# Performance work log

Hardware: AMD Instinct MI355X
Metric: run time of the kernel (lower is better)

Reference implementation:

```python
import jax, jax.numpy as jnp
import numpy as np

N, M, NNZ, D, H = 4096, 1024, 65536, 512, 8
DH = D // H
DFF = 4 * D
EPS = 1e-5


def layer_norm(x, g, b):
    mu = jnp.mean(x, axis=-1, keepdims=True)
    var = jnp.mean((x - mu) ** 2, axis=-1, keepdims=True)
    return (x - mu) / jnp.sqrt(var + EPS) * g + b


def setup_inputs() -> dict:
    key = jax.random.key(0)
    ks = jax.random.split(key, 16)
    s = 1.0 / np.sqrt(D)
    inp = {}
    inp['x'] = jax.random.normal(ks[0], (N, D), jnp.float32)
    node = jax.random.randint(ks[1], (NNZ,), 0, N, jnp.int32)
    edge = jax.random.randint(ks[2], (NNZ,), 0, M, jnp.int32)
    inp['hyperedge_index'] = jnp.stack([node, edge], axis=0)
    inp['hyperedge_attr'] = jax.random.normal(ks[3], (M, D), jnp.float32)
    # HypergraphConv params (heads=1): lin (no bias), att [2*D], output bias
    inp['Wh'] = jax.random.normal(ks[4], (D, D), jnp.float32) * s
    inp['att'] = jax.random.normal(ks[5], (2 * D,), jnp.float32) * s
    inp['bias_h'] = jnp.zeros((D,), jnp.float32)
    # outer LayerNorms
    inp['ln1_g'] = jnp.ones((D,), jnp.float32); inp['ln1_b'] = jnp.zeros((D,), jnp.float32)
    inp['ln2_g'] = jnp.ones((D,), jnp.float32); inp['ln2_b'] = jnp.zeros((D,), jnp.float32)
    # TransformerEncoderLayer params (post-norm, relu, dropout off at eval)
    inp['in_proj_w'] = jax.random.normal(ks[6], (3 * D, D), jnp.float32) * s
    inp['in_proj_b'] = jnp.zeros((3 * D,), jnp.float32)
    inp['out_proj_w'] = jax.random.normal(ks[7], (D, D), jnp.float32) * s
    inp['out_proj_b'] = jnp.zeros((D,), jnp.float32)
    inp['ff1_w'] = jax.random.normal(ks[8], (DFF, D), jnp.float32) * s
    inp['ff1_b'] = jnp.zeros((DFF,), jnp.float32)
    inp['ff2_w'] = jax.random.normal(ks[9], (D, DFF), jnp.float32) * (1.0 / np.sqrt(DFF))
    inp['ff2_b'] = jnp.zeros((D,), jnp.float32)
    inp['tln1_g'] = jnp.ones((D,), jnp.float32); inp['tln1_b'] = jnp.zeros((D,), jnp.float32)
    inp['tln2_g'] = jnp.ones((D,), jnp.float32); inp['tln2_b'] = jnp.zeros((D,), jnp.float32)
    return inp


def hypergraph_conv(x, node, edge, hyperedge_attr, Wh, att, bias_h):
    # PyG HypergraphConv, use_attention=True, heads=1, concat=True
    xl = x @ Wh.T                      # [N, D]
    el = hyperedge_attr @ Wh.T         # [M, D]
    # per-incidence attention score
    a = xl[node] @ att[:D] + el[edge] @ att[D:]          # [NNZ]
    a = jnp.where(a >= 0, a, 0.2 * a)                    # leaky_relu(0.2)
    # scatter-softmax grouped by node index
    amax = jax.ops.segment_max(a, node, num_segments=N)
    a = jnp.exp(a - amax[node])
    den = jax.ops.segment_sum(a, node, num_segments=N)
    alpha = a / (den[node] + 1e-16)
    # degree normalizations (hyperedge_weight = ones)
    ones = jnp.ones((NNZ,), x.dtype)
    Dn = jax.ops.segment_sum(ones, node, num_segments=N)
    Dinv = jnp.where(Dn > 0, 1.0 / Dn, 0.0)
    Bn = jax.ops.segment_sum(ones, edge, num_segments=M)
    Binv = jnp.where(Bn > 0, 1.0 / Bn, 0.0)
    # node -> hyperedge aggregation
    msg1 = (Binv[edge] * alpha)[:, None] * xl[node]      # [NNZ, D]
    ef = jax.ops.segment_sum(msg1, edge, num_segments=M)  # [M, D]
    # hyperedge -> node aggregation
    msg2 = (Dinv[node] * alpha)[:, None] * ef[edge]
    out = jax.ops.segment_sum(msg2, node, num_segments=N)  # [N, D]
    return out + bias_h


def reference(x, hyperedge_index, hyperedge_attr, Wh, att, bias_h,
              ln1_g, ln1_b, ln2_g, ln2_b,
              in_proj_w, in_proj_b, out_proj_w, out_proj_b,
              ff1_w, ff1_b, ff2_w, ff2_b,
              tln1_g, tln1_b, tln2_g, tln2_b):
    node, edge = hyperedge_index[0], hyperedge_index[1]
    x_conv = hypergraph_conv(x, node, edge, hyperedge_attr, Wh, att, bias_h)
    x1 = layer_norm(x + x_conv, ln1_g, ln1_b)
    # TransformerEncoderLayer (post-norm, eval: dropout off), seq of N tokens
    qkv = x1 @ in_proj_w.T + in_proj_b
    q, k, v = jnp.split(qkv, 3, axis=-1)
    q = q.reshape(N, H, DH); k = k.reshape(N, H, DH); v = v.reshape(N, H, DH)
    scores = jnp.einsum('nhd,mhd->hnm', q, k) / np.sqrt(DH)
    attw = jax.nn.softmax(scores, axis=-1)
    ctx = jnp.einsum('hnm,mhd->nhd', attw, v).reshape(N, D)
    attn_out = ctx @ out_proj_w.T + out_proj_b
    x2 = layer_norm(x1 + attn_out, tln1_g, tln1_b)
    ff = jax.nn.relu(x2 @ ff1_w.T + ff1_b) @ ff2_w.T + ff2_b
    x3 = layer_norm(x2 + ff, tln2_g, tln2_b)
    return layer_norm(x1 + x3, ln2_g, ln2_b)
```

## Files before the change

kernel.cpp:

```cpp
#include <hip/hip_runtime.h>
#include <math.h>

#define NN   4096
#define MM   1024
#define NNZC 65536
#define DD   512
#define HH   8
#define DHH  64
#define DFFC 2048
#define NSPLIT 8

typedef short bf16x8 __attribute__((ext_vector_type(8)));
typedef float f32x4  __attribute__((ext_vector_type(4)));

static __device__ inline unsigned short f2bf(float f) {
  union { float f; unsigned int u; } v; v.f = f;
  unsigned int r = v.u + 0x7fff + ((v.u >> 16) & 1);
  return (unsigned short)(r >> 16);
}
static __device__ inline float bf2f(unsigned short u) {
  return __uint_as_float((unsigned int)u << 16);
}

__device__ inline void gload16(const void* g, void* l) {
  __builtin_amdgcn_global_load_lds(
      (const __attribute__((address_space(1))) void*)g,
      (__attribute__((address_space(3))) void*)l, 16, 0, 0);
}

__device__ inline void atomicMaxF(float* addr, float val) {
  if (val >= 0.f) atomicMax((int*)addr, __float_as_int(val));
  else            atomicMin((unsigned int*)addr, __float_as_uint(val));
}

__global__ void init_kernel(float* amax, float* den, int* DnCnt, int* BnCnt,
                            int* node_cur, int* edge_cur) {
  int i = blockIdx.x * 256 + threadIdx.x;
  if (i < NN) { amax[i] = -INFINITY; den[i] = 0.f; DnCnt[i] = 0; node_cur[i] = 0; }
  if (i < MM) { BnCnt[i] = 0; edge_cur[i] = 0; }
}

__global__ __launch_bounds__(256) void f2b_multi(
    const float* s0, unsigned short* d0, int n0,
    const float* s1, unsigned short* d1, int n1,
    const float* s2, unsigned short* d2, int n2,
    const float* s3, unsigned short* d3, int n3,
    const float* s4, unsigned short* d4, int n4,
    const float* s5, unsigned short* d5, int n5,
    const float* s6, unsigned short* d6, int n6) {
  const float* in; unsigned short* out; int n8;
  switch (blockIdx.y) {
    case 0: in=s0; out=d0; n8=n0; break;
    case 1: in=s1; out=d1; n8=n1; break;
    case 2: in=s2; out=d2; n8=n2; break;
    case 3: in=s3; out=d3; n8=n3; break;
    case 4: in=s4; out=d4; n8=n4; break;
    case 5: in=s5; out=d5; n8=n5; break;
    default: in=s6; out=d6; n8=n6; break;
  }
  for (int i = blockIdx.x*256 + threadIdx.x; i < n8; i += gridDim.x*256) {
    float4 v0 = *(const float4*)&in[(size_t)i*8];
    float4 v1 = *(const float4*)&in[(size_t)i*8 + 4];
    unsigned short w[8];
    w[0]=f2bf(v0.x); w[1]=f2bf(v0.y); w[2]=f2bf(v0.z); w[3]=f2bf(v0.w);
    w[4]=f2bf(v1.x); w[5]=f2bf(v1.y); w[6]=f2bf(v1.z); w[7]=f2bf(v1.w);
    *(ulonglong2*)&out[(size_t)i*8] = *(ulonglong2*)w;
  }
}

__global__ __launch_bounds__(256) void gemm_bt_bf16(
    const unsigned short* __restrict__ A, const unsigned short* __restrict__ B,
    const float* __restrict__ bias, float* __restrict__ Cf,
    unsigned short* __restrict__ Cb, int N, int K, int relu) {
  __shared__ __align__(16) unsigned short Al[128*64];
  __shared__ __align__(16) unsigned short Bl[128*64];
  const int t = threadIdx.x;
  const int w = t >> 6, l = t & 63;
  const int lg = l >> 4, lid = l & 15;
  const int wr = w >> 1, wc = w & 1;
  const int bm = blockIdx.x * 128, bn = blockIdx.y * 128;

  f32x4 acc[4][4];
  #pragma unroll
  for (int mi = 0; mi < 4; ++mi)
    #pragma unroll
    for (int ni = 0; ni < 4; ++ni) acc[mi][ni] = (f32x4)0.f;

  for (int k0 = 0; k0 < K; k0 += 64) {
    #pragma unroll
    for (int i = 0; i < 4; ++i) {
      int cid = i*256 + t;
      int row = cid >> 3, cp = cid & 7;
      int gc = cp ^ (row & 7);
      gload16(&A[(size_t)(bm + row)*K + k0 + gc*8], &Al[cid*8]);
      gload16(&B[(size_t)(bn + row)*K + k0 + gc*8], &Bl[cid*8]);
    }
    asm volatile("s_waitcnt vmcnt(0)" ::: "memory");
    __syncthreads();
    #pragma unroll
    for (int ks = 0; ks < 2; ++ks) {
      bf16x8 af[4], bfr[4];
      #pragma unroll
      for (int mi = 0; mi < 4; ++mi) {
        int r = wr*64 + mi*16 + lid;
        af[mi] = *(const bf16x8*)&Al[r*64 + ((ks*4 + lg) ^ (r & 7))*8];
      }
      #pragma unroll
      for (int ni = 0; ni < 4; ++ni) {
        int r = wc*64 + ni*16 + lid;
        bfr[ni] = *(const bf16x8*)&Bl[r*64 + ((ks*4 + lg) ^ (r & 7))*8];
      }
      __builtin_amdgcn_s_setprio(1);
      #pragma unroll
      for (int mi = 0; mi < 4; ++mi)
        #pragma unroll
        for (int ni = 0; ni < 4; ++ni)
          acc[mi][ni] = __builtin_amdgcn_mfma_f32_16x16x32_bf16(af[mi], bfr[ni], acc[mi][ni], 0, 0, 0);
      __builtin_amdgcn_s_setprio(0);
    }
    __syncthreads();
  }

  #pragma unroll
  for (int ni = 0; ni < 4; ++ni) {
    int col = bn + wc*64 + ni*16 + lid;
    float bv = bias ? bias[col] : 0.f;
    #pragma unroll
    for (int mi = 0; mi < 4; ++mi) {
      #pragma unroll
      for (int rg = 0; rg < 4; ++rg) {
        int row = bm + wr*64 + mi*16 + lg*4 + rg;
        float v = acc[mi][ni][rg] + bv;
        if (relu) v = fmaxf(v, 0.f);
        if (Cf) Cf[(size_t)row*N + col] = v;
        if (Cb) Cb[(size_t)row*N + col] = f2bf(v);
      }
    }
  }
}

__global__ __launch_bounds__(256) void gemm_bt_bf16_n64(
    const unsigned short* __restrict__ A, const unsigned short* __restrict__ B,
    const float* __restrict__ bias, unsigned short* __restrict__ Cb, int N, int K,
    unsigned short* __restrict__ VtbOpt) {
  __shared__ __align__(16) unsigned short Al[128*64];
  __shared__ __align__(16) unsigned short Bl[64*64];
  const int t = threadIdx.x;
  const int w = t >> 6, l = t & 63;
  const int lg = l >> 4, lid = l & 15;
  const int wr = w >> 1, wc = w & 1;
  const int bm = blockIdx.x * 128, bn = blockIdx.y * 64;

  f32x4 acc[4][2];
  #pragma unroll
  for (int mi = 0; mi < 4; ++mi)
    #pragma unroll
    for (int ni = 0; ni < 2; ++ni) acc[mi][ni] = (f32x4)0.f;

  for (int k0 = 0; k0 < K; k0 += 64) {
    #pragma unroll
    for (int i = 0; i < 4; ++i) {
      int cid = i*256 + t;
      int row = cid >> 3, cp = cid & 7;
      int gc = cp ^ (row & 7);
      gload16(&A[(size_t)(bm + row)*K + k0 + gc*8], &Al[cid*8]);
    }
    #pragma unroll
    for (int i = 0; i < 2; ++i) {
      int cid = i*256 + t;
      int row = cid >> 3, cp = cid & 7;
      int gc = cp ^ (row & 7);
      gload16(&B[(size_t)(bn + row)*K + k0 + gc*8], &Bl[cid*8]);
    }
    asm volatile("s_waitcnt vmcnt(0)" ::: "memory");
    __syncthreads();
    #pragma unroll
    for (int ks = 0; ks < 2; ++ks) {
      bf16x8 af[4], bfr[2];
      #pragma unroll
      for (int mi = 0; mi < 4; ++mi) {
        int r = wr*64 + mi*16 + lid;
        af[mi] = *(const bf16x8*)&Al[r*64 + ((ks*4 + lg) ^ (r & 7))*8];
      }
      #pragma unroll
      for (int ni = 0; ni < 2; ++ni) {
        int r = wc*32 + ni*16 + lid;
        bfr[ni] = *(const bf16x8*)&Bl[r*64 + ((ks*4 + lg) ^ (r & 7))*8];
      }
      __builtin_amdgcn_s_setprio(1);
      #pragma unroll
      for (int mi = 0; mi < 4; ++mi)
        #pragma unroll
        for (int ni = 0; ni < 2; ++ni)
          acc[mi][ni] = __builtin_amdgcn_mfma_f32_16x16x32_bf16(af[mi], bfr[ni], acc[mi][ni], 0, 0, 0);
      __builtin_amdgcn_s_setprio(0);
    }
    __syncthreads();
  }

  if (VtbOpt && bn >= 1024) {
    #pragma unroll
    for (int ni = 0; ni < 2; ++ni) {
      int col = bn + wc*32 + ni*16 + lid;
      float bv = bias ? bias[col] : 0.f;
      int d = col - 1024;
      int h = d >> 6, dd = d & 63;
      #pragma unroll
      for (int mi = 0; mi < 4; ++mi) {
        int tok0 = bm + wr*64 + mi*16 + lg*4;
        ushort4 w4;
        w4.x = f2bf(acc[mi][ni][0] + bv);
        w4.y = f2bf(acc[mi][ni][1] + bv);
        w4.z = f2bf(acc[mi][ni][2] + bv);
        w4.w = f2bf(acc[mi][ni][3] + bv);
        *(ushort4*)&VtbOpt[(size_t)h*64*NN + (size_t)dd*NN + tok0] = w4;
      }
    }
  } else {
    #pragma unroll
    for (int ni = 0; ni < 2; ++ni) {
      int col = bn + wc*32 + ni*16 + lid;
      float bv = bias ? bias[col] : 0.f;
      #pragma unroll
      for (int mi = 0; mi < 4; ++mi) {
        #pragma unroll
        for (int rg = 0; rg < 4; ++rg) {
          int row = bm + wr*64 + mi*16 + lg*4 + rg;
          Cb[(size_t)row*N + col] = f2bf(acc[mi][ni][rg] + bv);
        }
      }
    }
  }
}

__global__ __launch_bounds__(256) void rowdot_both(const unsigned short* __restrict__ xlb,
    const unsigned short* __restrict__ elb, const float* __restrict__ att,
    float* __restrict__ s_node, float* __restrict__ s_edge) {
  int w = (blockIdx.x * 256 + threadIdx.x) >> 6;
  int lane = threadIdx.x & 63;
  const unsigned short* xr;
  const float* vec;
  if (w < NN) { xr = &xlb[(size_t)w * DD]; vec = att; }
  else        { xr = &elb[(size_t)(w - NN) * DD]; vec = att + DD; }
  float s = 0.f;
  #pragma unroll
  for (int j = 0; j < 8; ++j) s += bf2f(xr[lane + 64*j]) * vec[lane + 64*j];
  #pragma unroll
  for (int off = 1; off < 64; off <<= 1) s += __shfl_xor(s, off, 64);
  if (lane == 0) {
    if (w < NN) s_node[w] = s;
    else        s_edge[w - NN] = s;
  }
}

__global__ void incidence_pass1(const int* __restrict__ node_idx, const int* __restrict__ edge_idx,
    const float* __restrict__ s_node, const float* __restrict__ s_edge,
    float* __restrict__ a_buf, float* amax, int* DnCnt, int* BnCnt) {
  int i = blockIdx.x * 256 + threadIdx.x;
  if (i >= NNZC) return;
  int n = node_idx[i], m = edge_idx[i];
  float a = s_node[n] + s_edge[m];
  a = (a >= 0.f) ? a : 0.2f * a;
  a_buf[i] = a;
  atomicMaxF(&amax[n], a);
  atomicAdd(&DnCnt[n], 1);
  atomicAdd(&BnCnt[m], 1);
}

__global__ __launch_bounds__(1024) void exscan2_kernel(const int* __restrict__ inA,
    int* __restrict__ outA, int nA, const int* __restrict__ inB, int* __restrict__ outB, int nB) {
  const int* in; int* out; int n;
  if (blockIdx.x == 0) { in = inA; out = outA; n = nA; }
  else                 { in = inB; out = outB; n = nB; }
  __shared__ int sums[1024];
  const int t = threadIdx.x;
  const int chunk = (n + 1023) >> 10;
  const int start = t * chunk;
  const int stop  = min(start + chunk, n);
  int local = 0;
  for (int i = start; i < stop; ++i) local += in[i];
  sums[t] = local;
  __syncthreads();
  for (int o = 1; o < 1024; o <<= 1) {
    int v = (t >= o) ? sums[t - o] : 0;
    __syncthreads();
    sums[t] += v;
    __syncthreads();
  }
  int run = (t == 0) ? 0 : sums[t - 1];
  for (int i = start; i < stop; ++i) { out[i] = run; run += in[i]; }
  if (t == 1023) out[n] = sums[1023];
}

__global__ void incidence_pass2(const int* __restrict__ node_idx, const int* __restrict__ edge_idx,
    float* __restrict__ a_buf, const float* __restrict__ amax, float* den,
    const int* __restrict__ node_off, const int* __restrict__ edge_off,
    int* node_cur, int* edge_cur, int* node_list, int* edge_list) {
  int i = blockIdx.x * 256 + threadIdx.x;
  if (i >= NNZC) return;
  int n = node_idx[i], m = edge_idx[i];
  float e = __expf(a_buf[i] - amax[n]);
  a_buf[i] = e;
  atomicAdd(&den[n], e);
  int pn = atomicAdd(&node_cur[n], 1);
  node_list[node_off[n] + pn] = i;
  int pm = atomicAdd(&edge_cur[m], 1);
  edge_list[edge_off[m] + pm] = i;
}

__global__ __launch_bounds__(256) void gather_edge(const int* __restrict__ edge_off,
    const int* __restrict__ edge_list, const int* __restrict__ node_idx,
    const float* __restrict__ a_buf, const float* __restrict__ den,
    const unsigned short* __restrict__ xlb, unsigned short* __restrict__ efb) {
  int m = blockIdx.x;
  int t = threadIdx.x;
  int beg = edge_off[m], end = edge_off[m+1];
  int cnt = end - beg;
  float Binv = (cnt > 0) ? (1.0f / (float)cnt) : 0.f;
  __shared__ int   ln_[128];
  __shared__ float lw_[128];
  float acc0 = 0.f, acc1 = 0.f;
  for (int c = beg; c < end; c += 128) {
    int nchunk = min(128, end - c);
    if (t < nchunk) {
      int i = edge_list[c + t];
      int n = node_idx[i];
      ln_[t] = n;
      lw_[t] = a_buf[i] / (den[n] + 1e-16f) * Binv;
    }
    __syncthreads();
    float a0 = 0.f, a1 = 0.f, b0 = 0.f, b1 = 0.f;
    int j = 0;
    for (; j + 1 < nchunk; j += 2) {
      float w0 = lw_[j], w1 = lw_[j+1];
      const unsigned short* r0 = &xlb[(size_t)ln_[j]   * DD];
      const unsigned short* r1 = &xlb[(size_t)ln_[j+1] * DD];
      a0 += w0 * bf2f(r0[t]);       b0 += w0 * bf2f(r0[t + 256]);
      a1 += w1 * bf2f(r1[t]);       b1 += w1 * bf2f(r1[t + 256]);
    }
    if (j < nchunk) {
      float w0 = lw_[j];
      const unsigned short* r0 = &xlb[(size_t)ln_[j] * DD];
      a0 += w0 * bf2f(r0[t]);       b0 += w0 * bf2f(r0[t + 256]);
    }
    acc0 += a0 + a1;
    acc1 += b0 + b1;
    __syncthreads();
  }
  efb[(size_t)m * DD + t]       = f2bf(acc0);
  efb[(size_t)m * DD + t + 256] = f2bf(acc1);
}

__global__ __launch_bounds__(256) void gather_node_ln(const int* __restrict__ node_off,
    const int* __restrict__ node_list, const int* __restrict__ edge_idx,
    const float* __restrict__ a_buf, const float* __restrict__ den,
    const unsigned short* __restrict__ efb, const float* __restrict__ bias_h,
    const float* __restrict__ x, const float* __restrict__ g, const float* __restrict__ be,
    float* __restrict__ x1, unsigned short* __restrict__ x1b) {
  int n = blockIdx.x;
  int t = threadIdx.x;
  int beg = node_off[n], end = node_off[n+1];
  int cnt = end - beg;
  float Dinv = (cnt > 0) ? (1.0f / (float)cnt) : 0.f;
  float wscale = Dinv / (den[n] + 1e-16f);
  __shared__ int   le_[128];
  __shared__ float lw_[128];
  float acc0 = 0.f, acc1 = 0.f;
  for (int c = beg; c < end; c += 128) {
    int nchunk = min(128, end - c);
    if (t < nchunk) {
      int i = node_list[c + t];
      le_[t] = edge_idx[i];
      lw_[t] = a_buf[i] * wscale;
    }
    __syncthreads();
    float a0 = 0.f, a1 = 0.f, b0 = 0.f, b1 = 0.f;
    int j = 0;
    for (; j + 1 < nchunk; j += 2) {
      float w0 = lw_[j], w1 = lw_[j+1];
      const unsigned short* r0 = &efb[(size_t)le_[j]   * DD];
      const unsigned short* r1 = &efb[(size_t)le_[j+1] * DD];
      a0 += w0 * bf2f(r0[t]);       b0 += w0 * bf2f(r0[t + 256]);
      a1 += w1 * bf2f(r1[t]);       b1 += w1 * bf2f(r1[t + 256]);
    }
    if (j < nchunk) {
      float w0 = lw_[j];
      const unsigned short* r0 = &efb[(size_t)le_[j] * DD];
      a0 += w0 * bf2f(r0[t]);       b0 += w0 * bf2f(r0[t + 256]);
    }
    acc0 += a0 + a1;
    acc1 += b0 + b1;
    __syncthreads();
  }
  float v0 = x[(size_t)n*DD + t]       + acc0 + bias_h[t];
  float v1 = x[(size_t)n*DD + t + 256] + acc1 + bias_h[t + 256];
  __shared__ float red[4];
  __shared__ float mu_s, rstd_s;
  float s = v0 + v1;
  #pragma unroll
  for (int off = 1; off < 64; off <<= 1) s += __shfl_xor(s, off, 64);
  int wid = t >> 6;
  if ((t & 63) == 0) red[wid] = s;
  __syncthreads();
  if (t == 0) mu_s = (red[0] + red[1] + red[2] + red[3]) / 512.f;
  __syncthreads();
  float mu = mu_s;
  float d0 = v0 - mu, d1 = v1 - mu;
  float vs = d0*d0 + d1*d1;
  #pragma unroll
  for (int off = 1; off < 64; off <<= 1) vs += __shfl_xor(vs, off, 64);
  if ((t & 63) == 0) red[wid] = vs;
  __syncthreads();
  if (t == 0) rstd_s = rsqrtf((red[0] + red[1] + red[2] + red[3]) / 512.f + 1e-5f);
  __syncthreads();
  float rs = rstd_s;
  float o0 = d0 * rs * g[t]       + be[t];
  float o1 = d1 * rs * g[t + 256] + be[t + 256];
  x1[(size_t)n*DD + t]        = o0;
  x1[(size_t)n*DD + t + 256]  = o1;
  x1b[(size_t)n*DD + t]       = f2bf(o0);
  x1b[(size_t)n*DD + t + 256] = f2bf(o1);
}

__global__ __launch_bounds__(256) void ln_residual(const float* __restrict__ a,
    const float* __restrict__ b, const unsigned short* __restrict__ bB,
    const float* __restrict__ g, const float* __restrict__ be,
    float* __restrict__ out, unsigned short* __restrict__ outb) {
  int r = blockIdx.x;
  int t = threadIdx.x;
  float b0 = b ? b[(size_t)r*DD + t]       : bf2f(bB[(size_t)r*DD + t]);
  float b1 = b ? b[(size_t)r*DD + t + 256] : bf2f(bB[(size_t)r*DD + t + 256]);
  float v0 = a[(size_t)r*DD + t]       + b0;
  float v1 = a[(size_t)r*DD + t + 256] + b1;
  __shared__ float red[4];
  __shared__ float mu_s, rstd_s;
  float s = v0 + v1;
  #pragma unroll
  for (int off = 1; off < 64; off <<= 1) s += __shfl_xor(s, off, 64);
  int wid = t >> 6;
  if ((t & 63) == 0) red[wid] = s;
  __syncthreads();
  if (t == 0) mu_s = (red[0] + red[1] + red[2] + red[3]) / 512.f;
  __syncthreads();
  float mu = mu_s;
  float d0 = v0 - mu, d1 = v1 - mu;
  float vs = d0*d0 + d1*d1;
  #pragma unroll
  for (int off = 1; off < 64; off <<= 1) vs += __shfl_xor(vs, off, 64);
  if ((t & 63) == 0) red[wid] = vs;
  __syncthreads();
  if (t == 0) rstd_s = rsqrtf((red[0] + red[1] + red[2] + red[3]) / 512.f + 1e-5f);
  __syncthreads();
  float rs = rstd_s;
  float o0 = d0 * rs * g[t]       + be[t];
  float o1 = d1 * rs * g[t + 256] + be[t + 256];
  out[(size_t)r*DD + t]       = o0;
  out[(size_t)r*DD + t + 256] = o1;
  if (outb) {
    outb[(size_t)r*DD + t]       = f2bf(o0);
    outb[(size_t)r*DD + t + 256] = f2bf(o1);
  }
}

__global__ __launch_bounds__(256) void ln_final2(const float* __restrict__ x2,
    const unsigned short* __restrict__ ffob, const float* __restrict__ x1,
    const float* __restrict__ g1, const float* __restrict__ b1,
    const float* __restrict__ g2, const float* __restrict__ b2,
    float* __restrict__ out) {
  int r = blockIdx.x;
  int t = threadIdx.x;
  __shared__ float red[4];
  __shared__ float sh0, sh1;
  int wid = t >> 6;
  float v0 = x2[(size_t)r*DD + t]       + bf2f(ffob[(size_t)r*DD + t]);
  float v1 = x2[(size_t)r*DD + t + 256] + bf2f(ffob[(size_t)r*DD + t + 256]);
  float s = v0 + v1;
  #pragma unroll
  for (int off = 1; off < 64; off <<= 1) s += __shfl_xor(s, off, 64);
  if ((t & 63) == 0) red[wid] = s;
  __syncthreads();
  if (t == 0) sh0 = (red[0] + red[1] + red[2] + red[3]) / 512.f;
  __syncthreads();
  float mu = sh0;
  float d0 = v0 - mu, d1 = v1 - mu;
  float vs = d0*d0 + d1*d1;
  #pragma unroll
  for (int off = 1; off < 64; off <<= 1) vs += __shfl_xor(vs, off, 64);
  if ((t & 63) == 0) red[wid] = vs;
  __syncthreads();
  if (t == 0) sh1 = rsqrtf((red[0] + red[1] + red[2] + red[3]) / 512.f + 1e-5f);
  __syncthreads();
  float rs = sh1;
  float x30 = d0 * rs * g1[t]       + b1[t];
  float x31 = d1 * rs * g1[t + 256] + b1[t + 256];
  __syncthreads();
  float u0 = x1[(size_t)r*DD + t]       + x30;
  float u1 = x1[(size_t)r*DD + t + 256] + x31;
  s = u0 + u1;
  #pragma unroll
  for (int off = 1; off < 64; off <<= 1) s += __shfl_xor(s, off, 64);
  if ((t & 63) == 0) red[wid] = s;
  __syncthreads();
  if (t == 0) sh0 = (red[0] + red[1] + red[2] + red[3]) / 512.f;
  __syncthreads();
  mu = sh0;
  d0 = u0 - mu; d1 = u1 - mu;
  vs = d0*d0 + d1*d1;
  #pragma unroll
  for (int off = 1; off < 64; off <<= 1) vs += __shfl_xor(vs, off, 64);
  if ((t & 63) == 0) red[wid] = vs;
  __syncthreads();
  if (t == 0) sh1 = rsqrtf((red[0] + red[1] + red[2] + red[3]) / 512.f + 1e-5f);
  __syncthreads();
  rs = sh1;
  out[(size_t)r*DD + t]       = d0 * rs * g2[t]       + b2[t];
  out[(size_t)r*DD + t + 256] = d1 * rs * g2[t + 256] + b2[t + 256];
}

__global__ __launch_bounds__(256) void attn_mfma_part(const unsigned short* __restrict__ qkvbb,
                                                      const unsigned short* __restrict__ Vtb,
                                                      unsigned short* __restrict__ Opartb,
                                                      float* __restrict__ ml) {
  const int head = blockIdx.y;
  const int z = blockIdx.z;
  const int q0 = blockIdx.x * 64;
  const int t = threadIdx.x;
  const int w = t >> 6;
  const int l = t & 63;
  const int lg = l >> 4;
  const int lid = l & 15;
  const float sc = 0.125f * 1.44269504f;
  const float THRraw = 44.36f;

  __shared__ __align__(16) unsigned short Kl[64*64];
  __shared__ __align__(16) unsigned short Vl[64*64];

  bf16x8 qa[2];
  {
    const int qrow = q0 + w*16 + lid;
    const unsigned short* qp = &qkvbb[(size_t)qrow*1536 + head*64];
    qa[0] = *(const bf16x8*)&qp[lg*8];
    qa[1] = *(const bf16x8*)&qp[32 + lg*8];
  }

  float m = -1e30f, msc = -1e30f, lsum = 0.f;
  f32x4 o[4];
  #pragma unroll
  for (int dt = 0; dt < 4; ++dt) o[dt] = (f32x4)0.f;

  const unsigned short* Kh = qkvbb + 512 + head*64;
  const unsigned short* Vh = Vtb + (size_t)head*64*NN;
  const int kt0 = z * (NN / NSPLIT);
  const int kt1 = kt0 + (NN / NSPLIT);

  const int srow0 = t >> 3,        scc = (t & 7) * 8;
  const int srow1 = 32 + (t >> 3);
  const int sdst0 = (srow0*64 + scc) ^ ((srow0 & 7) << 3);
  const int sdst1 = (srow1*64 + scc) ^ ((srow1 & 7) << 3);
  const int kperm0 = 8*((srow0>>2)&3) + 4*((srow0>>4)&1) + (srow0&3) + 32*(srow0>>5);
  const int kperm1 = 8*((srow1>>2)&3) + 4*((srow1>>4)&1) + (srow1&3) + 32*(srow1>>5);
  ulonglong2 kreg0, kreg1, vreg0, vreg1;

#define LOADKV(ktv) do { \
    kreg0 = *(const ulonglong2*)&Kh[(size_t)((ktv) + kperm0)*1536 + scc]; \
    vreg0 = *(const ulonglong2*)&Vh[(size_t)srow0*NN + (ktv) + scc]; \
    kreg1 = *(const ulonglong2*)&Kh[(size_t)((ktv) + kperm1)*1536 + scc]; \
    vreg1 = *(const ulonglong2*)&Vh[(size_t)srow1*NN + (ktv) + scc]; \
  } while (0)
#define STORKV() do { \
    *(ulonglong2*)&Kl[sdst0] = kreg0; *(ulonglong2*)&Vl[sdst0] = vreg0; \
    *(ulonglong2*)&Kl[sdst1] = kreg1; *(ulonglong2*)&Vl[sdst1] = vreg1; \
  } while (0)

  LOADKV(kt0);
  STORKV();
  __syncthreads();

  for (int kt = kt0; kt < kt1; kt += 64) {
    const bool hn = (kt + 64) < kt1;
    if (hn) LOADKV(kt + 64);

    f32x4 s[4];
    #pragma unroll
    for (int n = 0; n < 4; ++n) s[n] = (f32x4)0.f;
    __builtin_amdgcn_s_setprio(1);
    #pragma unroll
    for (int n = 0; n < 4; ++n) {
      int tok = n*16 + lid;
      #pragma unroll
      for (int hf = 0; hf < 2; ++hf) {
        int didx = (tok*64 + hf*32 + lg*8) ^ ((tok & 7) << 3);
        bf16x8 kb = *(const bf16x8*)&Kl[didx];
        s[n] = __builtin_amdgcn_mfma_f32_16x16x32_bf16(kb, qa[hf], s[n], 0, 0, 0);
      }
    }
    __builtin_amdgcn_s_setprio(0);

    float a0 = fmaxf(fmaxf(s[0][0], s[0][1]), s[0][2]);
    float a1 = fmaxf(fmaxf(s[0][3], s[1][0]), s[1][1]);
    float a2 = fmaxf(fmaxf(s[1][2], s[1][3]), s[2][0]);
    float a3 = fmaxf(fmaxf(s[2][1], s[2][2]), s[2][3]);
    float a4 = fmaxf(fmaxf(s[3][0], s[3][1]), s[3][2]);
    float mx = fmaxf(fmaxf(fmaxf(a0, a1), a2), fmaxf(fmaxf(a3, a4), s[3][3]));
    mx = fmaxf(mx, __shfl_xor(mx, 16, 64));
    mx = fmaxf(mx, __shfl_xor(mx, 32, 64));
    if (!__all(mx <= m + THRraw)) {
      float mn = fmaxf(m, mx);
      float c = exp2f((m - mn) * sc);
      m = mn;
      msc = m * sc;
      lsum *= c;
      #pragma unroll
      for (int r = 0; r < 4; ++r) {
        float cr = __shfl(c, lg*4 + r, 64);
        #pragma unroll
        for (int dt = 0; dt < 4; ++dt) o[dt][r] *= cr;
      }
    }
    float ps = 0.f;
    #pragma unroll
    for (int n = 0; n < 4; ++n)
      #pragma unroll
      for (int r = 0; r < 4; ++r) {
        float p = exp2f(fmaf(s[n][r], sc, -msc));
        s[n][r] = p;
        ps += p;
      }
    ps += __shfl_xor(ps, 16, 64);
    ps += __shfl_xor(ps, 32, 64);
    lsum += ps;

    union { bf16x8 v; unsigned int u[4]; } pa[2];
    #pragma unroll
    for (int hf = 0; hf < 2; ++hf) {
      asm("v_cvt_pk_bf16_f32 %0, %1, %2" : "=v"(pa[hf].u[0]) : "v"(s[2*hf][0]),   "v"(s[2*hf][1]));
      asm("v_cvt_pk_bf16_f32 %0, %1, %2" : "=v"(pa[hf].u[1]) : "v"(s[2*hf][2]),   "v"(s[2*hf][3]));
      asm("v_cvt_pk_bf16_f32 %0, %1, %2" : "=v"(pa[hf].u[2]) : "v"(s[2*hf+1][0]), "v"(s[2*hf+1][1]));
      asm("v_cvt_pk_bf16_f32 %0, %1, %2" : "=v"(pa[hf].u[3]) : "v"(s[2*hf+1][2]), "v"(s[2*hf+1][3]));
    }

    __builtin_amdgcn_s_setprio(1);
    #pragma unroll
    for (int dt = 0; dt < 4; ++dt) {
      int drow = dt*16 + lid;
      #pragma unroll
      for (int hf = 0; hf < 2; ++hf) {
        int didx = (drow*64 + hf*32 + lg*8) ^ ((drow & 7) << 3);
        bf16x8 vb = *(const bf16x8*)&Vl[didx];
        o[dt] = __builtin_amdgcn_mfma_f32_16x16x32_bf16(pa[hf].v, vb, o[dt], 0, 0, 0);
      }
    }
    __builtin_amdgcn_s_setprio(0);

    __syncthreads();
    if (hn) {
      STORKV();
      __syncthreads();
    }
  }
#undef LOADKV
#undef STORKV

  #pragma unroll
  for (int r = 0; r < 4; ++r) {
    int q = q0 + w*16 + lg*4 + r;
    size_t base = ((size_t)(z*HH + head)*NN + q)*64;
    #pragma unroll
    for (int dt = 0; dt < 4; ++dt)
      Opartb[base + dt*16 + lid] = f2bf(o[dt][r]);
  }
  if (l < 16) {
    int q = q0 + w*16 + l;
    size_t mb = ((size_t)(z*HH + head)*NN + q)*2;
    ml[mb]     = msc;
    ml[mb + 1] = lsum;
  }
}

__global__ __launch_bounds__(256) void attn_combine(const unsigned short* __restrict__ Opartb,
                                                    const float* __restrict__ ml,
                                                    unsigned short* __restrict__ ctxb) {
  const int w = threadIdx.x >> 6, lane = threadIdx.x & 63;
  const int row = blockIdx.x * 4 + w;
  const int q = row >> 3, head = row & 7;
  float ms[NSPLIT], ls[NSPLIT];
  float mglob = -1e30f;
  #pragma unroll
  for (int s = 0; s < NSPLIT; ++s) {
    size_t mb = ((size_t)(s*HH + head)*NN + q)*2;
    ms[s] = ml[mb]; ls[s] = ml[mb + 1];
    mglob = fmaxf(mglob, ms[s]);
  }
  float lt = 0.f, ov = 0.f;
  #pragma unroll
  for (int s = 0; s < NSPLIT; ++s) {
    float wgt = exp2f(ms[s] - mglob);
    lt += ls[s] * wgt;
    ov += bf2f(Opartb[((size_t)(s*HH + head)*NN + q)*64 + lane]) * wgt;
  }
  ctxb[(size_t)q*DD + head*64 + lane] = f2bf(ov / lt);
}

extern "C" void kernel_launch(void* const* d_in, const int* in_sizes, int n_in,
                              void* d_out, int out_size, void* d_ws, size_t ws_size,
                              hipStream_t stream) {
  const float* x       = (const float*)d_in[0];
  const int*   hidx    = (const int*)d_in[1];
  const float* hattr   = (const float*)d_in[2];
  const float* Wh      = (const float*)d_in[3];
  const float* att     = (const float*)d_in[4];
  const float* bias_h  = (const float*)d_in[5];
  const float* ln1_g   = (const float*)d_in[6];
  const float* ln1_b   = (const float*)d_in[7];
  const float* ln2_g   = (const float*)d_in[8];
  const float* ln2_b   = (const float*)d_in[9];
  const float* in_proj_w  = (const float*)d_in[10];
  const float* in_proj_b  = (const float*)d_in[11];
  const float* out_proj_w = (const float*)d_in[12];
  const float* out_proj_b = (const float*)d_in[13];
  const float* ff1_w   = (const float*)d_in[14];
  const float* ff1_b   = (const float*)d_in[15];
  const float* ff2_w   = (const float*)d_in[16];
  const float* ff2_b   = (const float*)d_in[17];
  const float* tln1_g  = (const float*)d_in[18];
  const float* tln1_b  = (const float*)d_in[19];
  const float* tln2_g  = (const float*)d_in[20];
  const float* tln2_b  = (const float*)d_in[21];
  const int* node_idx = hidx;
  const int* edge_idx = hidx + NNZC;

  char* ws = (char*)d_ws;
  size_t off = 0;
  auto alloc = [&](size_t bytes) -> void* {
    void* p = ws + off;
    off = (off + bytes + 63) & ~(size_t)63;
    return p;
  };
  float* s_node   = (float*)alloc(sizeof(float)*NN);
  float* s_edge   = (float*)alloc(sizeof(float)*MM);
  float* a_buf    = (float*)alloc(sizeof(float)*NNZC);
  float* amax     = (float*)alloc(sizeof(float)*NN);
  float* den      = (float*)alloc(sizeof(float)*NN);
  int*   DnCnt    = (int*)alloc(sizeof(int)*NN);
  int*   BnCnt    = (int*)alloc(sizeof(int)*MM);
  int*   node_off = (int*)alloc(sizeof(int)*(NN+1));
  int*   edge_off = (int*)alloc(sizeof(int)*(MM+1));
  int*   node_cur = (int*)alloc(sizeof(int)*NN);
  int*   edge_cur = (int*)alloc(sizeof(int)*MM);
  int*   node_list= (int*)alloc(sizeof(int)*NNZC);
  int*   edge_list= (int*)alloc(sizeof(int)*NNZC);
  float* x1       = (float*)alloc(sizeof(float)*NN*DD);
  float* x2       = (float*)alloc(sizeof(float)*NN*DD);
  unsigned short* xhb   = (unsigned short*)alloc(sizeof(unsigned short)*(NN+MM)*DD);
  unsigned short* xelb  = (unsigned short*)alloc(sizeof(unsigned short)*(NN+MM)*DD);
  unsigned short* efb   = (unsigned short*)alloc(sizeof(unsigned short)*MM*DD);
  unsigned short* qkvbb = (unsigned short*)alloc(sizeof(unsigned short)*NN*3*DD);
  unsigned short* Vtb   = (unsigned short*)alloc(sizeof(unsigned short)*NN*DD);
  unsigned short* Whb   = (unsigned short*)alloc(sizeof(unsigned short)*DD*DD);
  unsigned short* ipwb  = (unsigned short*)alloc(sizeof(unsigned short)*3*DD*DD);
  unsigned short* opwb  = (unsigned short*)alloc(sizeof(unsigned short)*DD*DD);
  unsigned short* ff1wb = (unsigned short*)alloc(sizeof(unsigned short)*DFFC*DD);
  unsigned short* ff2wb = (unsigned short*)alloc(sizeof(unsigned short)*DD*DFFC);
  unsigned short* x1b   = (unsigned short*)alloc(sizeof(unsigned short)*NN*DD);
  unsigned short* x2b   = (unsigned short*)alloc(sizeof(unsigned short)*NN*DD);
  unsigned short* ctxb  = (unsigned short*)alloc(sizeof(unsigned short)*NN*DD);
  unsigned short* attn_outb = (unsigned short*)alloc(sizeof(unsigned short)*NN*DD);
  char* late = (char*)alloc(34u*1024*1024);
  unsigned short* Opartb = (unsigned short*)late;
  float*          mlb    = (float*)(late + 32u*1024*1024);
  unsigned short* ffhb   = (unsigned short*)late;
  unsigned short* ffob   = (unsigned short*)(late + 16u*1024*1024);
  unsigned short* xlb = xelb;
  unsigned short* elb = xelb + (size_t)NN*DD;
  (void)ws_size; (void)in_sizes; (void)n_in; (void)out_size;

  dim3 b256(256);
  f2b_multi<<<dim3(256, 7), b256, 0, stream>>>(
      x, xhb, NN*DD/8,  hattr, xhb + (size_t)NN*DD, MM*DD/8,  Wh, Whb, DD*DD/8,
      in_proj_w, ipwb, 3*DD*DD/8,  out_proj_w, opwb, DD*DD/8,
      ff1_w, ff1wb, DFFC*DD/8,  ff2_w, ff2wb, DD*DFFC/8);

  gemm_bt_bf16_n64<<<dim3((NN+MM)/128, DD/64), b256, 0, stream>>>(xhb, Whb, nullptr, xelb, DD, DD, nullptr);
  rowdot_both<<<(NN+MM)/4, b256, 0, stream>>>(xlb, elb, att, s_node, s_edge);
  init_kernel<<<NN/256, b256, 0, stream>>>(amax, den, DnCnt, BnCnt, node_cur, edge_cur);
  incidence_pass1<<<NNZC/256, b256, 0, stream>>>(node_idx, edge_idx, s_node, s_edge,
                                                 a_buf, amax, DnCnt, BnCnt);
  exscan2_kernel<<<2, 1024, 0, stream>>>(DnCnt, node_off, NN, BnCnt, edge_off, MM);
  incidence_pass2<<<NNZC/256, b256, 0, stream>>>(node_idx, edge_idx, a_buf, amax, den,
                                                 node_off, edge_off, node_cur, edge_cur,
                                                 node_list, edge_list);
  gather_edge<<<MM, b256, 0, stream>>>(edge_off, edge_list, node_idx, a_buf, den, xlb, efb);
  gather_node_ln<<<NN, b256, 0, stream>>>(node_off, node_list, edge_idx, a_buf, den, efb,
                                          bias_h, x, ln1_g, ln1_b, x1, x1b);
  gemm_bt_bf16_n64<<<dim3(NN/128, (3*DD)/64), b256, 0, stream>>>(x1b, ipwb, in_proj_b, qkvbb, 3*DD, DD, Vtb);
  attn_mfma_part<<<dim3(NN/64, HH, NSPLIT), b256, 0, stream>>>(qkvbb, Vtb, Opartb, mlb);
  attn_combine<<<NN*HH/4, b256, 0, stream>>>(Opartb, mlb, ctxb);
  gemm_bt_bf16_n64<<<dim3(NN/128, DD/64), b256, 0, stream>>>(ctxb, opwb, out_proj_b, attn_outb, DD, DD, nullptr);
  ln_residual<<<NN, b256, 0, stream>>>(x1, nullptr, attn_outb, tln1_g, tln1_b, x2, x2b);
  gemm_bt_bf16<<<dim3(NN/128, DFFC/128), b256, 0, stream>>>(x2b, ff1wb, ff1_b, nullptr, ffhb, DFFC, DD, 1);
  gemm_bt_bf16_n64<<<dim3(NN/128, DD/64), b256, 0, stream>>>(ffhb, ff2wb, ff2_b, ffob, DD, DFFC, nullptr);
  ln_final2<<<NN, b256, 0, stream>>>(x2, ffob, x1, tln2_g, tln2_b, ln2_g, ln2_b, (float*)d_out);
}
```

Baseline: 271.8 us.

## Drop fp32 residual copies, halve attention split-K, precompute LDS swizzle addresses

Removes the fp32 x1/x2 intermediates so the layer norms read and write only bf16 residuals, reducing global memory traffic. Halves the attention KV split count, which shrinks the partial-output buffer and the combine work but gives each block more serial work and fewer blocks. Precomputes swizzled LDS addresses for K/V fragment loads outside the loop. The residual path now carries bf16 rounding, which lowers accuracy.

Result: faster. 264.4 us (-2.7%).

```diff
diff --git a/kernel.cpp b/kernel.cpp
--- a/kernel.cpp
+++ b/kernel.cpp
@@ -8,7 +8,7 @@
 #define HH   8
 #define DHH  64
 #define DFFC 2048
-#define NSPLIT 8
+#define NSPLIT 4
 
 typedef short bf16x8 __attribute__((ext_vector_type(8)));
 typedef float f32x4  __attribute__((ext_vector_type(4)));
@@ -356,7 +356,7 @@
     const float* __restrict__ a_buf, const float* __restrict__ den,
     const unsigned short* __restrict__ efb, const float* __restrict__ bias_h,
     const float* __restrict__ x, const float* __restrict__ g, const float* __restrict__ be,
-    float* __restrict__ x1, unsigned short* __restrict__ x1b) {
+    unsigned short* __restrict__ x1b) {
   int n = blockIdx.x;
   int t = threadIdx.x;
   int beg = node_off[n], end = node_off[n+1];
@@ -414,24 +414,17 @@
   if (t == 0) rstd_s = rsqrtf((red[0] + red[1] + red[2] + red[3]) / 512.f + 1e-5f);
   __syncthreads();
   float rs = rstd_s;
-  float o0 = d0 * rs * g[t]       + be[t];
-  float o1 = d1 * rs * g[t + 256] + be[t + 256];
-  x1[(size_t)n*DD + t]        = o0;
-  x1[(size_t)n*DD + t + 256]  = o1;
-  x1b[(size_t)n*DD + t]       = f2bf(o0);
-  x1b[(size_t)n*DD + t + 256] = f2bf(o1);
-}
-
-__global__ __launch_bounds__(256) void ln_residual(const float* __restrict__ a,
-    const float* __restrict__ b, const unsigned short* __restrict__ bB,
-    const float* __restrict__ g, const float* __restrict__ be,
-    float* __restrict__ out, unsigned short* __restrict__ outb) {
+  x1b[(size_t)n*DD + t]       = f2bf(d0 * rs * g[t]       + be[t]);
+  x1b[(size_t)n*DD + t + 256] = f2bf(d1 * rs * g[t + 256] + be[t + 256]);
+}
+
+__global__ __launch_bounds__(256) void ln_res_bb(const unsigned short* __restrict__ a,
+    const unsigned short* __restrict__ b, const float* __restrict__ g,
+    const float* __restrict__ be, unsigned short* __restrict__ outb) {
   int r = blockIdx.x;
   int t = threadIdx.x;
-  float b0 = b ? b[(size_t)r*DD + t]       : bf2f(bB[(size_t)r*DD + t]);
-  float b1 = b ? b[(size_t)r*DD + t + 256] : bf2f(bB[(size_t)r*DD + t + 256]);
-  float v0 = a[(size_t)r*DD + t]       + b0;
-  float v1 = a[(size_t)r*DD + t + 256] + b1;
+  float v0 = bf2f(a[(size_t)r*DD + t])       + bf2f(b[(size_t)r*DD + t]);
+  float v1 = bf2f(a[(size_t)r*DD + t + 256]) + bf2f(b[(size_t)r*DD + t + 256]);
   __shared__ float red[4];
   __shared__ float mu_s, rstd_s;
   float s = v0 + v1;
@@ -452,18 +445,12 @@
   if (t == 0) rstd_s = rsqrtf((red[0] + red[1] + red[2] + red[3]) / 512.f + 1e-5f);
   __syncthreads();
   float rs = rstd_s;
-  float o0 = d0 * rs * g[t]       + be[t];
-  float o1 = d1 * rs * g[t + 256] + be[t + 256];
-  out[(size_t)r*DD + t]       = o0;
-  out[(size_t)r*DD + t + 256] = o1;
-  if (outb) {
-    outb[(size_t)r*DD + t]       = f2bf(o0);
-    outb[(size_t)r*DD + t + 256] = f2bf(o1);
-  }
-}
-
-__global__ __launch_bounds__(256) void ln_final2(const float* __restrict__ x2,
-    const unsigned short* __restrict__ ffob, const float* __restrict__ x1,
+  outb[(size_t)r*DD + t]       = f2bf(d0 * rs * g[t]       + be[t]);
+  outb[(size_t)r*DD + t + 256] = f2bf(d1 * rs * g[t + 256] + be[t + 256]);
+}
+
+__global__ __launch_bounds__(256) void ln_final2(const unsigned short* __restrict__ x2b,
+    const unsigned short* __restrict__ ffob, const unsigned short* __restrict__ x1b,
     const float* __restrict__ g1, const float* __restrict__ b1,
     const float* __restrict__ g2, const float* __restrict__ b2,
     float* __restrict__ out) {
@@ -472,8 +459,8 @@
   __shared__ float red[4];
   __shared__ float sh0, sh1;
   int wid = t >> 6;
-  float v0 = x2[(size_t)r*DD + t]       + bf2f(ffob[(size_t)r*DD + t]);
-  float v1 = x2[(size_t)r*DD + t + 256] + bf2f(ffob[(size_t)r*DD + t + 256]);
+  float v0 = bf2f(x2b[(size_t)r*DD + t])       + bf2f(ffob[(size_t)r*DD + t]);
+  float v1 = bf2f(x2b[(size_t)r*DD + t + 256]) + bf2f(ffob[(size_t)r*DD + t + 256]);
   float s = v0 + v1;
   #pragma unroll
   for (int off = 1; off < 64; off <<= 1) s += __shfl_xor(s, off, 64);
@@ -494,8 +481,8 @@
   float x30 = d0 * rs * g1[t]       + b1[t];
   float x31 = d1 * rs * g1[t + 256] + b1[t + 256];
   __syncthreads();
-  float u0 = x1[(size_t)r*DD + t]       + x30;
-  float u1 = x1[(size_t)r*DD + t + 256] + x31;
+  float u0 = bf2f(x1b[(size_t)r*DD + t])       + x30;
+  float u1 = bf2f(x1b[(size_t)r*DD + t + 256]) + x31;
   s = u0 + u1;
   #pragma unroll
   for (int off = 1; off < 64; off <<= 1) s += __shfl_xor(s, off, 64);
@@ -543,6 +530,15 @@
     qa[1] = *(const bf16x8*)&qp[32 + lg*8];
   }
 
+  int addr[4][2];
+  #pragma unroll
+  for (int i = 0; i < 4; ++i)
+    #pragma unroll
+    for (int hf = 0; hf < 2; ++hf) {
+      int row = i*16 + lid;
+      addr[i][hf] = (row*64 + hf*32 + lg*8) ^ ((row & 7) << 3);
+    }
+
   float m = -1e30f, msc = -1e30f, lsum = 0.f;
   f32x4 o[4];
   #pragma unroll
@@ -586,11 +582,9 @@
     __builtin_amdgcn_s_setprio(1);
     #pragma unroll
     for (int n = 0; n < 4; ++n) {
-      int tok = n*16 + lid;
       #pragma unroll
       for (int hf = 0; hf < 2; ++hf) {
-        int didx = (tok*64 + hf*32 + lg*8) ^ ((tok & 7) << 3);
-        bf16x8 kb = *(const bf16x8*)&Kl[didx];
+        bf16x8 kb = *(const bf16x8*)&Kl[addr[n][hf]];
         s[n] = __builtin_amdgcn_mfma_f32_16x16x32_bf16(kb, qa[hf], s[n], 0, 0, 0);
       }
     }
@@ -642,11 +636,9 @@
     __builtin_amdgcn_s_setprio(1);
     #pragma unroll
     for (int dt = 0; dt < 4; ++dt) {
-      int drow = dt*16 + lid;
       #pragma unroll
       for (int hf = 0; hf < 2; ++hf) {
-        int didx = (drow*64 + hf*32 + lg*8) ^ ((drow & 7) << 3);
-        bf16x8 vb = *(const bf16x8*)&Vl[didx];
+        bf16x8 vb = *(const bf16x8*)&Vl[addr[dt][hf]];
         o[dt] = __builtin_amdgcn_mfma_f32_16x16x32_bf16(pa[hf].v, vb, o[dt], 0, 0, 0);
       }
     }
@@ -749,8 +741,6 @@
   int*   edge_cur = (int*)alloc(sizeof(int)*MM);
   int*   node_list= (int*)alloc(sizeof(int)*NNZC);
   int*   edge_list= (int*)alloc(sizeof(int)*NNZC);
-  float* x1       = (float*)alloc(sizeof(float)*NN*DD);
-  float* x2       = (float*)alloc(sizeof(float)*NN*DD);
   unsigned short* xhb   = (unsigned short*)alloc(sizeof(unsigned short)*(NN+MM)*DD);
   unsigned short* xelb  = (unsigned short*)alloc(sizeof(unsigned short)*(NN+MM)*DD);
   unsigned short* efb   = (unsigned short*)alloc(sizeof(unsigned short)*MM*DD);
@@ -765,9 +755,9 @@
   unsigned short* x2b   = (unsigned short*)alloc(sizeof(unsigned short)*NN*DD);
   unsigned short* ctxb  = (unsigned short*)alloc(sizeof(unsigned short)*NN*DD);
   unsigned short* attn_outb = (unsigned short*)alloc(sizeof(unsigned short)*NN*DD);
-  char* late = (char*)alloc(34u*1024*1024);
+  char* late = (char*)alloc(20u*1024*1024);
   unsigned short* Opartb = (unsigned short*)late;
-  float*          mlb    = (float*)(late + 32u*1024*1024);
+  float*          mlb    = (float*)(late + 16u*1024*1024);
   unsigned short* ffhb   = (unsigned short*)late;
   unsigned short* ffob   = (unsigned short*)(late + 16u*1024*1024);
   unsigned short* xlb = xelb;
@@ -791,13 +781,13 @@
                                                  node_list, edge_list);
   gather_edge<<<MM, b256, 0, stream>>>(edge_off, edge_list, node_idx, a_buf, den, xlb, efb);
   gather_node_ln<<<NN, b256, 0, stream>>>(node_off, node_list, edge_idx, a_buf, den, efb,
-                                          bias_h, x, ln1_g, ln1_b, x1, x1b);
+                                          bias_h, x, ln1_g, ln1_b, x1b);
   gemm_bt_bf16_n64<<<dim3(NN/128, (3*DD)/64), b256, 0, stream>>>(x1b, ipwb, in_proj_b, qkvbb, 3*DD, DD, Vtb);
   attn_mfma_part<<<dim3(NN/64, HH, NSPLIT), b256, 0, stream>>>(qkvbb, Vtb, Opartb, mlb);
   attn_combine<<<NN*HH/4, b256, 0, stream>>>(Opartb, mlb, ctxb);
   gemm_bt_bf16_n64<<<dim3(NN/128, DD/64), b256, 0, stream>>>(ctxb, opwb, out_proj_b, attn_outb, DD, DD, nullptr);
-  ln_residual<<<NN, b256, 0, stream>>>(x1, nullptr, attn_outb, tln1_g, tln1_b, x2, x2b);
+  ln_res_bb<<<NN, b256, 0, stream>>>(x1b, attn_outb, tln1_g, tln1_b, x2b);
   gemm_bt_bf16<<<dim3(NN/128, DFFC/128), b256, 0, stream>>>(x2b, ff1wb, ff1_b, nullptr, ffhb, DFFC, DD, 1);
   gemm_bt_bf16_n64<<<dim3(NN/128, DD/64), b256, 0, stream>>>(ffhb, ff2wb, ff2_b, ffob, DD, DFFC, nullptr);
-  ln_final2<<<NN, b256, 0, stream>>>(x2, ffob, x1, tln2_g, tln2_b, ln2_g, ln2_b, (float*)d_out);
-}
+  ln_final2<<<NN, b256, 0, stream>>>(x2b, ffob, x1b, tln2_g, tln2_b, ln2_g, ln2_b, (float*)d_out);
+}
```
